# Performance work log

Hardware: AMD Instinct MI355X
Metric: run time of the kernel (lower is better)

Reference implementation:

```python
import jax, jax.numpy as jnp
import numpy as np

N_NODES = 100000
N_EDGES = 3200000
D = 128


def setup_inputs() -> dict:
    key = jax.random.key(0)
    ks = jax.random.split(key, 6)
    x = jax.random.normal(ks[0], (N_NODES, D), dtype=jnp.float32)
    w = jax.random.uniform(ks[1], (N_EDGES,), dtype=jnp.float32)
    W = jax.random.normal(ks[2], (D, D), dtype=jnp.float32) * (1.0 / np.sqrt(D))
    b = jax.random.normal(ks[3], (D,), dtype=jnp.float32) * 0.01
    src = jax.random.randint(ks[4], (N_EDGES,), 0, N_NODES, dtype=jnp.int64)
    dst = jax.random.randint(ks[5], (N_EDGES,), 0, N_NODES, dtype=jnp.int64)
    return {"x": x, "w": w, "W": W, "b": b, "src": src, "dst": dst}


def reference(x, w, W, b, src, dst):
    # h = linear(x)  -> [N, D]
    h = x @ W.T + b
    # u_mul_e: gather source features, scale by per-edge weight  -> [E, D]
    m = h[src] * w[:, None]
    # sum aggregation at destinations (SpMM scatter-add)  -> [N, D]
    out = jax.ops.segment_sum(m, dst, num_segments=N_NODES)
    return out
```

## Files before the change

kernel.cpp:

```cpp
#include <hip/hip_runtime.h>
#include <hip/hip_fp16.h>

constexpr int N_NODES = 100000;
constexpr int N_EDGES = 3200000;
constexpr int NB2 = (N_NODES + 63) >> 6;
constexpr int LCAP = 2432;
constexpr int TILE = 8192;
constexpr int NTILES = (N_EDGES + TILE - 1) / TILE;
constexpr int NWIN = 8;
constexpr int NKEY = NWIN * 64;

__global__ __launch_bounds__(256) void cvt_kernel(const float* __restrict__ x,
                                                  __half* __restrict__ xh) {
  const int stride = gridDim.x * 256;
  const int total = N_NODES * 128 / 4;
  for (int i = blockIdx.x * 256 + threadIdx.x; i < total; i += stride) {
    float4 v = ((const float4*)x)[i];
    ((__half2*)xh)[2 * i] = __floats2half2_rn(v.x, v.y);
    ((__half2*)xh)[2 * i + 1] = __floats2half2_rn(v.z, v.w);
  }
}

__global__ __launch_bounds__(1024) void bin4_kernel(
    const int* __restrict__ src, const int* __restrict__ dst,
    const float* __restrict__ w, int* __restrict__ gtail,
    int2* __restrict__ lists) {
  __shared__ int lcnt[NB2];
  __shared__ int lbase[NB2];
  const int t = threadIdx.x;
  const int e0 = blockIdx.x * TILE;
  const int n = min(TILE, N_EDGES - e0);

  for (int i = t; i < NB2; i += 1024) lcnt[i] = 0;
  __syncthreads();

  for (int off = t; off < n; off += 1024)
    atomicAdd(&lcnt[(dst[e0 + off] >> 6)], 1);
  __syncthreads();

  for (int i = t; i < NB2; i += 1024) {
    int c = lcnt[i];
    lbase[i] = (c > 0) ? atomicAdd(&gtail[i], c) : 0;
    lcnt[i] = 0;
  }
  __syncthreads();

  for (int off = t; off < n; off += 1024) {
    int e = e0 + off;
    int d = dst[e];
    int l = d >> 6;
    int p = lbase[l] + atomicAdd(&lcnt[l], 1);
    if ((unsigned)p < (unsigned)LCAP)
      lists[(size_t)l * LCAP + p] =
          make_int2(src[e] | ((d & 63) << 17), __float_as_int(w[e]));
  }
}

__global__ __launch_bounds__(256) void agg5_kernel(
    const __half* __restrict__ xh, const int2* __restrict__ lists,
    const int* __restrict__ gtail, float* __restrict__ agg_out,
    float* __restrict__ sw) {
  __shared__ int2 sorted[LCAP];
  __shared__ int kcnt[NKEY];
  __shared__ int koff[NKEY + 1];
  __shared__ int kcur[NKEY];
  const int b = blockIdx.x;
  const int t = threadIdx.x;
  const int c = min(gtail[b], LCAP);
  const int2* base = lists + (size_t)b * LCAP;

  for (int i = t; i < NKEY; i += 256) kcnt[i] = 0;
  __syncthreads();

  for (int j = t; j < c; j += 256) {
    int rx = base[j].x;
    int key = ((rx & 0x1FFFF) >> 14) * 64 + ((rx >> 17) & 63);
    atomicAdd(&kcnt[key], 1);
  }
  __syncthreads();

  if (t < 64) {
    int base8 = t * 8;
    int loc[8], run = 0;
    #pragma unroll
    for (int i = 0; i < 8; ++i) { loc[i] = run; run += kcnt[base8 + i]; }
    int inc = run;
    #pragma unroll
    for (int d = 1; d < 64; d <<= 1) {
      int u = __shfl_up(inc, d, 64);
      if (t >= d) inc += u;
    }
    int excl = inc - run;
    #pragma unroll
    for (int i = 0; i < 8; ++i) {
      koff[base8 + i] = excl + loc[i];
      kcur[base8 + i] = excl + loc[i];
    }
    if (t == 63) koff[NKEY] = inc;
  }
  __syncthreads();

  for (int j = t; j < c; j += 256) {
    int2 r = base[j];
    int key = ((r.x & 0x1FFFF) >> 14) * 64 + ((r.x >> 17) & 63);
    int p = atomicAdd(&kcur[key], 1);
    if ((unsigned)p < (unsigned)LCAP) sorted[p] = r;
  }
  __syncthreads();

  const int wv = t >> 6, lane = t & 63;
  const int nd = min(64, N_NODES - b * 64);
  const __half2* xh2 = (const __half2*)xh;
  float2 acc[16];
  float sws[16];
  #pragma unroll
  for (int i = 0; i < 16; ++i) { acc[i] = make_float2(0.f, 0.f); sws[i] = 0.f; }

  for (int s = 0; s < NWIN; ++s) {
    #pragma unroll
    for (int ri = 0; ri < 16; ++ri) {
      int key = s * 64 + wv * 16 + ri;
      int j0 = min(koff[key], c), j1 = min(koff[key + 1], c);
      int j = j0;
      for (; j + 4 <= j1; j += 4) {
        int2 e0 = sorted[j];
        int2 e1 = sorted[j + 1];
        int2 e2 = sorted[j + 2];
        int2 e3 = sorted[j + 3];
        float2 v0 = __half22float2(xh2[(size_t)(e0.x & 0x1FFFF) * 64 + lane]);
        float2 v1 = __half22float2(xh2[(size_t)(e1.x & 0x1FFFF) * 64 + lane]);
        float2 v2 = __half22float2(xh2[(size_t)(e2.x & 0x1FFFF) * 64 + lane]);
        float2 v3 = __half22float2(xh2[(size_t)(e3.x & 0x1FFFF) * 64 + lane]);
        float w0 = __int_as_float(e0.y), w1 = __int_as_float(e1.y);
        float w2 = __int_as_float(e2.y), w3 = __int_as_float(e3.y);
        acc[ri].x = fmaf(w0, v0.x, acc[ri].x); acc[ri].y = fmaf(w0, v0.y, acc[ri].y);
        acc[ri].x = fmaf(w1, v1.x, acc[ri].x); acc[ri].y = fmaf(w1, v1.y, acc[ri].y);
        acc[ri].x = fmaf(w2, v2.x, acc[ri].x); acc[ri].y = fmaf(w2, v2.y, acc[ri].y);
        acc[ri].x = fmaf(w3, v3.x, acc[ri].x); acc[ri].y = fmaf(w3, v3.y, acc[ri].y);
        sws[ri] += (w0 + w1) + (w2 + w3);
      }
      for (; j < j1; ++j) {
        int2 e0 = sorted[j];
        float2 v0 = __half22float2(xh2[(size_t)(e0.x & 0x1FFFF) * 64 + lane]);
        float w0 = __int_as_float(e0.y);
        acc[ri].x = fmaf(w0, v0.x, acc[ri].x);
        acc[ri].y = fmaf(w0, v0.y, acc[ri].y);
        sws[ri] += w0;
      }
    }
  }

  #pragma unroll
  for (int ri = 0; ri < 16; ++ri) {
    int r = wv * 16 + ri;
    if (r < nd) {
      ((float2*)agg_out)[(size_t)(b * 64 + r) * 64 + lane] = acc[ri];
      if (lane == 0) sw[b * 64 + r] = sws[ri];
    }
  }
}

__global__ __launch_bounds__(256, 2) void linear3_kernel(
    float* __restrict__ io, const float* __restrict__ W,
    const float* __restrict__ bias, const float* __restrict__ sw) {
  __shared__ float Wt[128][132];
  const int t = threadIdx.x;
  const int row0 = blockIdx.x * 64;

  #pragma unroll
  for (int i = 0; i < 16; ++i) {
    int f4 = t + 256 * i;
    int c = f4 >> 5;
    int k = (f4 & 31) * 4;
    float4 v = *(const float4*)(W + (size_t)c * 128 + k);
    Wt[k + 0][c] = v.x;
    Wt[k + 1][c] = v.y;
    Wt[k + 2][c] = v.z;
    Wt[k + 3][c] = v.w;
  }
  __syncthreads();

  const int tx = t & 15;
  const int ty = t >> 4;
  const float* xr[4];
  #pragma unroll
  for (int i = 0; i < 4; ++i) {
    int r = row0 + ty * 4 + i;
    xr[i] = (r < N_NODES) ? (io + (size_t)r * 128) : io;
  }

  float acc[4][8];
  #pragma unroll
  for (int i = 0; i < 4; ++i)
    #pragma unroll
    for (int j = 0; j < 8; ++j) acc[i][j] = 0.f;

  for (int k0 = 0; k0 < 128; k0 += 4) {
    float4 a[4];
    #pragma unroll
    for (int i = 0; i < 4; ++i) a[i] = *(const float4*)(xr[i] + k0);
    #pragma unroll
    for (int kk = 0; kk < 4; ++kk) {
      int k = k0 + kk;
      float4 b0 = *(const float4*)&Wt[k][tx * 8];
      float4 b1 = *(const float4*)&Wt[k][tx * 8 + 4];
      #pragma unroll
      for (int i = 0; i < 4; ++i) {
        float av = (kk == 0) ? a[i].x : (kk == 1) ? a[i].y
                  : (kk == 2) ? a[i].z : a[i].w;
        acc[i][0] = fmaf(av, b0.x, acc[i][0]);
        acc[i][1] = fmaf(av, b0.y, acc[i][1]);
        acc[i][2] = fmaf(av, b0.z, acc[i][2]);
        acc[i][3] = fmaf(av, b0.w, acc[i][3]);
        acc[i][4] = fmaf(av, b1.x, acc[i][4]);
        acc[i][5] = fmaf(av, b1.y, acc[i][5]);
        acc[i][6] = fmaf(av, b1.z, acc[i][6]);
        acc[i][7] = fmaf(av, b1.w, acc[i][7]);
      }
    }
  }

  float4 bb0 = *(const float4*)(bias + tx * 8);
  float4 bb1 = *(const float4*)(bias + tx * 8 + 4);
  #pragma unroll
  for (int i = 0; i < 4; ++i) {
    int r = row0 + ty * 4 + i;
    if (r < N_NODES) {
      float s = sw[r];
      float4 o0 = make_float4(acc[i][0] + s * bb0.x, acc[i][1] + s * bb0.y,
                              acc[i][2] + s * bb0.z, acc[i][3] + s * bb0.w);
      float4 o1 = make_float4(acc[i][4] + s * bb1.x, acc[i][5] + s * bb1.y,
                              acc[i][6] + s * bb1.z, acc[i][7] + s * bb1.w);
      float* orow = io + (size_t)r * 128 + tx * 8;
      *(float4*)orow = o0;
      *(float4*)(orow + 4) = o1;
    }
  }
}

extern "C" void kernel_launch(void* const* d_in, const int* in_sizes, int n_in,
                              void* d_out, int out_size, void* d_ws, size_t ws_size,
                              hipStream_t stream) {
  const float* x = (const float*)d_in[0];
  const float* w = (const float*)d_in[1];
  const float* W = (const float*)d_in[2];
  const float* bias = (const float*)d_in[3];
  const int* src = (const int*)d_in[4];
  const int* dst = (const int*)d_in[5];
  float* out = (float*)d_out;

  char* p = (char*)d_ws;
  __half* xh = (__half*)p;
  size_t o = (size_t)N_NODES * 128 * sizeof(__half);
  o = (o + 255) & ~(size_t)255;
  int2* lists = (int2*)(p + o);
  o += (size_t)NB2 * LCAP * sizeof(int2);
  int* gtail = (int*)(p + o);
  o += (size_t)NB2 * sizeof(int);
  o = (o + 255) & ~(size_t)255;
  float* sw = (float*)(p + o);

  hipMemsetAsync(gtail, 0, (size_t)NB2 * sizeof(int), stream);
  cvt_kernel<<<2048, 256, 0, stream>>>(x, xh);
  bin4_kernel<<<NTILES, 1024, 0, stream>>>(src, dst, w, gtail, lists);
  agg5_kernel<<<NB2, 256, 0, stream>>>(xh, lists, gtail, out, sw);
  linear3_kernel<<<NB2, 256, 0, stream>>>(out, W, bias, sw);
}
```

Baseline: 483.4 us.

## Stage binned edges in LDS for coalesced list writes and reorder agg keys

The binning kernel now computes per-bucket offsets with a block-wide scan, places records in shared memory sorted by bucket, and then writes them to the global lists in contiguous runs. This replaces scattered global writes with coalesced ones. The aggregation kernel's sort key now puts the destination row first and the source window second, so each row's edges are contiguous and processed in a single pass with one accumulator and an 8-way unrolled gather instead of 16 register accumulators over 8 windows. This lowers register pressure and per-window loop overhead, but uses about 130KB of LDS per bin block and weakens the source-window locality across rows.

New measurement: 390.9 us. -19.1%, faster.

```diff
diff --git a/kernel.cpp b/kernel.cpp
--- a/kernel.cpp
+++ b/kernel.cpp
@@ -5,10 +5,10 @@
 constexpr int N_EDGES = 3200000;
 constexpr int NB2 = (N_NODES + 63) >> 6;
 constexpr int LCAP = 2432;
-constexpr int TILE = 8192;
-constexpr int NTILES = (N_EDGES + TILE - 1) / TILE;
+constexpr int TILE2 = 12500;
+constexpr int NTILE2 = N_EDGES / TILE2;
 constexpr int NWIN = 8;
-constexpr int NKEY = NWIN * 64;
+constexpr int NKEY = 64 * NWIN;
 
 __global__ __launch_bounds__(256) void cvt_kernel(const float* __restrict__ x,
                                                   __half* __restrict__ xh) {
@@ -21,42 +21,83 @@
   }
 }
 
-__global__ __launch_bounds__(1024) void bin4_kernel(
+__global__ __launch_bounds__(1024) void bin5_kernel(
     const int* __restrict__ src, const int* __restrict__ dst,
     const float* __restrict__ w, int* __restrict__ gtail,
     int2* __restrict__ lists) {
+  __shared__ int2 rec[TILE2];
+  __shared__ unsigned short lid[TILE2];
   __shared__ int lcnt[NB2];
+  __shared__ int loff[NB2];
   __shared__ int lbase[NB2];
+  __shared__ int wsum[16];
   const int t = threadIdx.x;
-  const int e0 = blockIdx.x * TILE;
-  const int n = min(TILE, N_EDGES - e0);
+  const int e0 = blockIdx.x * TILE2;
 
   for (int i = t; i < NB2; i += 1024) lcnt[i] = 0;
   __syncthreads();
 
-  for (int off = t; off < n; off += 1024)
-    atomicAdd(&lcnt[(dst[e0 + off] >> 6)], 1);
+  for (int i = t; i < TILE2; i += 1024)
+    atomicAdd(&lcnt[dst[e0 + i] >> 6], 1);
+  __syncthreads();
+
+  {
+    int i0 = 2 * t, i1 = 2 * t + 1;
+    int c0 = (i0 < NB2) ? lcnt[i0] : 0;
+    int c1 = (i1 < NB2) ? lcnt[i1] : 0;
+    int v = c0 + c1;
+    int inc = v;
+    #pragma unroll
+    for (int d = 1; d < 64; d <<= 1) {
+      int u = __shfl_up(inc, d, 64);
+      if ((t & 63) >= d) inc += u;
+    }
+    if ((t & 63) == 63) wsum[t >> 6] = inc;
+    __syncthreads();
+    if (t < 16) {
+      int s = wsum[t];
+      int inc2 = s;
+      #pragma unroll
+      for (int d = 1; d < 16; d <<= 1) {
+        int u = __shfl_up(inc2, d, 64);
+        if (t >= d) inc2 += u;
+      }
+      wsum[t] = inc2 - s;
+    }
+    __syncthreads();
+    int excl = (inc - v) + wsum[t >> 6];
+    if (i0 < NB2) loff[i0] = excl;
+    if (i1 < NB2) loff[i1] = excl + c0;
+  }
   __syncthreads();
 
   for (int i = t; i < NB2; i += 1024) {
     int c = lcnt[i];
     lbase[i] = (c > 0) ? atomicAdd(&gtail[i], c) : 0;
-    lcnt[i] = 0;
-  }
-  __syncthreads();
-
-  for (int off = t; off < n; off += 1024) {
-    int e = e0 + off;
+  }
+  __syncthreads();
+  for (int i = t; i < NB2; i += 1024) lcnt[i] = loff[i];
+  __syncthreads();
+
+  for (int i = t; i < TILE2; i += 1024) {
+    int e = e0 + i;
     int d = dst[e];
     int l = d >> 6;
-    int p = lbase[l] + atomicAdd(&lcnt[l], 1);
-    if ((unsigned)p < (unsigned)LCAP)
-      lists[(size_t)l * LCAP + p] =
-          make_int2(src[e] | ((d & 63) << 17), __float_as_int(w[e]));
-  }
-}
-
-__global__ __launch_bounds__(256) void agg5_kernel(
+    int p = atomicAdd(&lcnt[l], 1);
+    rec[p] = make_int2(src[e] | ((d & 63) << 17), __float_as_int(w[e]));
+    lid[p] = (unsigned short)l;
+  }
+  __syncthreads();
+
+  for (int q = t; q < TILE2; q += 1024) {
+    int l = lid[q];
+    int dest = lbase[l] + (q - loff[l]);
+    if ((unsigned)dest < (unsigned)LCAP)
+      lists[(size_t)l * LCAP + dest] = rec[q];
+  }
+}
+
+__global__ __launch_bounds__(256) void agg6_kernel(
     const __half* __restrict__ xh, const int2* __restrict__ lists,
     const int* __restrict__ gtail, float* __restrict__ agg_out,
     float* __restrict__ sw) {
@@ -74,7 +115,7 @@
 
   for (int j = t; j < c; j += 256) {
     int rx = base[j].x;
-    int key = ((rx & 0x1FFFF) >> 14) * 64 + ((rx >> 17) & 63);
+    int key = ((rx >> 17) & 63) * 8 + ((rx & 0x1FFFF) >> 14);
     atomicAdd(&kcnt[key], 1);
   }
   __syncthreads();
@@ -102,7 +143,7 @@
 
   for (int j = t; j < c; j += 256) {
     int2 r = base[j];
-    int key = ((r.x & 0x1FFFF) >> 14) * 64 + ((r.x >> 17) & 63);
+    int key = ((r.x >> 17) & 63) * 8 + ((r.x & 0x1FFFF) >> 14);
     int p = atomicAdd(&kcur[key], 1);
     if ((unsigned)p < (unsigned)LCAP) sorted[p] = r;
   }
@@ -111,51 +152,54 @@
   const int wv = t >> 6, lane = t & 63;
   const int nd = min(64, N_NODES - b * 64);
   const __half2* xh2 = (const __half2*)xh;
-  float2 acc[16];
-  float sws[16];
-  #pragma unroll
-  for (int i = 0; i < 16; ++i) { acc[i] = make_float2(0.f, 0.f); sws[i] = 0.f; }
-
-  for (int s = 0; s < NWIN; ++s) {
-    #pragma unroll
-    for (int ri = 0; ri < 16; ++ri) {
-      int key = s * 64 + wv * 16 + ri;
-      int j0 = min(koff[key], c), j1 = min(koff[key + 1], c);
-      int j = j0;
-      for (; j + 4 <= j1; j += 4) {
-        int2 e0 = sorted[j];
-        int2 e1 = sorted[j + 1];
-        int2 e2 = sorted[j + 2];
-        int2 e3 = sorted[j + 3];
-        float2 v0 = __half22float2(xh2[(size_t)(e0.x & 0x1FFFF) * 64 + lane]);
-        float2 v1 = __half22float2(xh2[(size_t)(e1.x & 0x1FFFF) * 64 + lane]);
-        float2 v2 = __half22float2(xh2[(size_t)(e2.x & 0x1FFFF) * 64 + lane]);
-        float2 v3 = __half22float2(xh2[(size_t)(e3.x & 0x1FFFF) * 64 + lane]);
-        float w0 = __int_as_float(e0.y), w1 = __int_as_float(e1.y);
-        float w2 = __int_as_float(e2.y), w3 = __int_as_float(e3.y);
-        acc[ri].x = fmaf(w0, v0.x, acc[ri].x); acc[ri].y = fmaf(w0, v0.y, acc[ri].y);
-        acc[ri].x = fmaf(w1, v1.x, acc[ri].x); acc[ri].y = fmaf(w1, v1.y, acc[ri].y);
-        acc[ri].x = fmaf(w2, v2.x, acc[ri].x); acc[ri].y = fmaf(w2, v2.y, acc[ri].y);
-        acc[ri].x = fmaf(w3, v3.x, acc[ri].x); acc[ri].y = fmaf(w3, v3.y, acc[ri].y);
-        sws[ri] += (w0 + w1) + (w2 + w3);
-      }
-      for (; j < j1; ++j) {
-        int2 e0 = sorted[j];
-        float2 v0 = __half22float2(xh2[(size_t)(e0.x & 0x1FFFF) * 64 + lane]);
-        float w0 = __int_as_float(e0.y);
-        acc[ri].x = fmaf(w0, v0.x, acc[ri].x);
-        acc[ri].y = fmaf(w0, v0.y, acc[ri].y);
-        sws[ri] += w0;
-      }
-    }
-  }
-
-  #pragma unroll
   for (int ri = 0; ri < 16; ++ri) {
     int r = wv * 16 + ri;
+    int j0 = min(koff[r * 8], c), j1 = min(koff[r * 8 + 8], c);
+    float2 acc = make_float2(0.f, 0.f);
+    float sws = 0.f;
+    int j = j0;
+    for (; j + 8 <= j1; j += 8) {
+      int2 e0 = sorted[j];
+      int2 e1 = sorted[j + 1];
+      int2 e2 = sorted[j + 2];
+      int2 e3 = sorted[j + 3];
+      int2 e4 = sorted[j + 4];
+      int2 e5 = sorted[j + 5];
+      int2 e6 = sorted[j + 6];
+      int2 e7 = sorted[j + 7];
+      float2 v0 = __half22float2(xh2[(size_t)(e0.x & 0x1FFFF) * 64 + lane]);
+      float2 v1 = __half22float2(xh2[(size_t)(e1.x & 0x1FFFF) * 64 + lane]);
+      float2 v2 = __half22float2(xh2[(size_t)(e2.x & 0x1FFFF) * 64 + lane]);
+      float2 v3 = __half22float2(xh2[(size_t)(e3.x & 0x1FFFF) * 64 + lane]);
+      float2 v4 = __half22float2(xh2[(size_t)(e4.x & 0x1FFFF) * 64 + lane]);
+      float2 v5 = __half22float2(xh2[(size_t)(e5.x & 0x1FFFF) * 64 + lane]);
+      float2 v6 = __half22float2(xh2[(size_t)(e6.x & 0x1FFFF) * 64 + lane]);
+      float2 v7 = __half22float2(xh2[(size_t)(e7.x & 0x1FFFF) * 64 + lane]);
+      float w0 = __int_as_float(e0.y), w1 = __int_as_float(e1.y);
+      float w2 = __int_as_float(e2.y), w3 = __int_as_float(e3.y);
+      float w4 = __int_as_float(e4.y), w5 = __int_as_float(e5.y);
+      float w6 = __int_as_float(e6.y), w7 = __int_as_float(e7.y);
+      acc.x = fmaf(w0, v0.x, acc.x); acc.y = fmaf(w0, v0.y, acc.y);
+      acc.x = fmaf(w1, v1.x, acc.x); acc.y = fmaf(w1, v1.y, acc.y);
+      acc.x = fmaf(w2, v2.x, acc.x); acc.y = fmaf(w2, v2.y, acc.y);
+      acc.x = fmaf(w3, v3.x, acc.x); acc.y = fmaf(w3, v3.y, acc.y);
+      acc.x = fmaf(w4, v4.x, acc.x); acc.y = fmaf(w4, v4.y, acc.y);
+      acc.x = fmaf(w5, v5.x, acc.x); acc.y = fmaf(w5, v5.y, acc.y);
+      acc.x = fmaf(w6, v6.x, acc.x); acc.y = fmaf(w6, v6.y, acc.y);
+      acc.x = fmaf(w7, v7.x, acc.x); acc.y = fmaf(w7, v7.y, acc.y);
+      sws += ((w0 + w1) + (w2 + w3)) + ((w4 + w5) + (w6 + w7));
+    }
+    for (; j < j1; ++j) {
+      int2 e0 = sorted[j];
+      float2 v0 = __half22float2(xh2[(size_t)(e0.x & 0x1FFFF) * 64 + lane]);
+      float w0 = __int_as_float(e0.y);
+      acc.x = fmaf(w0, v0.x, acc.x);
+      acc.y = fmaf(w0, v0.y, acc.y);
+      sws += w0;
+    }
     if (r < nd) {
-      ((float2*)agg_out)[(size_t)(b * 64 + r) * 64 + lane] = acc[ri];
-      if (lane == 0) sw[b * 64 + r] = sws[ri];
+      ((float2*)agg_out)[(size_t)(b * 64 + r) * 64 + lane] = acc;
+      if (lane == 0) sw[b * 64 + r] = sws;
     }
   }
 }
@@ -262,7 +306,7 @@
 
   hipMemsetAsync(gtail, 0, (size_t)NB2 * sizeof(int), stream);
   cvt_kernel<<<2048, 256, 0, stream>>>(x, xh);
-  bin4_kernel<<<NTILES, 1024, 0, stream>>>(src, dst, w, gtail, lists);
-  agg5_kernel<<<NB2, 256, 0, stream>>>(xh, lists, gtail, out, sw);
+  bin5_kernel<<<NTILE2, 1024, 0, stream>>>(src, dst, w, gtail, lists);
+  agg6_kernel<<<NB2, 256, 0, stream>>>(xh, lists, gtail, out, sw);
   linear3_kernel<<<NB2, 256, 0, stream>>>(out, W, bias, sw);
 }
```
